# Kernel optimization log

Measured on AMD Instinct MI355X. Metric: run time of the kernel, lower is better.

## Reference

```python
import jax, jax.numpy as jnp
from jax import lax
import numpy as np

SEQ_LEN, INPUT_DIM, NUM_HIDDEN, NUM_CLASSES, BATCH = 512, 64, 128, 10, 1024


def setup_inputs() -> dict:
    key = jax.random.key(0)
    ks = jax.random.split(key, 12)
    bound = float(np.sqrt(1.0 / NUM_HIDDEN))

    def u(k, shape):
        return jax.random.uniform(k, shape, jnp.float32, -bound, bound)

    return {
        "x": jax.random.normal(ks[0], (BATCH, SEQ_LEN, INPUT_DIM), jnp.float32),
        "W_gx": u(ks[1], (INPUT_DIM, NUM_HIDDEN)),
        "W_gh": u(ks[2], (NUM_HIDDEN, NUM_HIDDEN)),
        "W_ix": u(ks[3], (INPUT_DIM, NUM_HIDDEN)),
        "W_ih": u(ks[4], (NUM_HIDDEN, NUM_HIDDEN)),
        "W_fx": u(ks[5], (INPUT_DIM, NUM_HIDDEN)),
        "W_fh": u(ks[6], (NUM_HIDDEN, NUM_HIDDEN)),
        "W_ox": u(ks[7], (INPUT_DIM, NUM_HIDDEN)),
        "W_oh": u(ks[8], (NUM_HIDDEN, NUM_HIDDEN)),
        "W_ph": u(ks[9], (NUM_HIDDEN, NUM_CLASSES)),
        "b_g": jnp.zeros((NUM_HIDDEN,), jnp.float32),
        "b_i": jnp.zeros((NUM_HIDDEN,), jnp.float32),
        "b_f": jnp.ones((NUM_HIDDEN,), jnp.float32),  # forget-gate bias init to 1 as in original
        "b_o": jnp.zeros((NUM_HIDDEN,), jnp.float32),
        "b_p": jnp.zeros((NUM_CLASSES,), jnp.float32),
    }


def reference(x, W_gx, W_gh, W_ix, W_ih, W_fx, W_fh, W_ox, W_oh, W_ph,
              b_g, b_i, b_f, b_o, b_p):
    B, T, D = x.shape
    H = W_gh.shape[0]

    def step(carry, x_t):  # x_t: [B, D]
        h, c = carry
        g = jnp.tanh(x_t @ W_gx + h @ W_gh + b_g)
        i = jax.nn.sigmoid(x_t @ W_ix + h @ W_ih + b_i)
        f = jax.nn.sigmoid(x_t @ W_fx + h @ W_fh + b_f)
        o = jax.nn.sigmoid(x_t @ W_ox + h @ W_oh + b_o)
        c = g * i + c * f
        h = jnp.tanh(c) * o
        return (h, c), None

    h0 = jnp.zeros((B, H), x.dtype)
    c0 = jnp.zeros((B, H), x.dtype)
    (h, c), _ = lax.scan(step, (h0, c0), jnp.swapaxes(x, 0, 1))  # scan over time
    return h @ W_ph + b_p  # [B, num_classes]
```

## Files before the change

### kernel.cpp

```cpp
#include <hip/hip_runtime.h>

#define BATCH 1024
#define TSEQ  512
#define DIN   64
#define H     128
#define NCLS  10
#define BM    16
#define NTHREADS 512

typedef _Float16 h16;
typedef __attribute__((ext_vector_type(4))) _Float16 half4v;
typedef __attribute__((ext_vector_type(8))) _Float16 half8v;
typedef __attribute__((ext_vector_type(4))) float f32x4;

__device__ __forceinline__ int stg_addr(int m, int k) {
    const int kg = k >> 3;
    return (((kg << 4) + (m ^ (kg & 7))) << 3) + (k & 7);
}

__device__ __forceinline__ half4v pack4(float a, float b, float c, float d) {
    half4v v;
    v[0] = (h16)a; v[1] = (h16)b; v[2] = (h16)c; v[3] = (h16)d;
    return v;
}

__device__ __forceinline__ float sig_f(float x) {
    return __builtin_amdgcn_rcpf(1.f + __builtin_amdgcn_exp2f(x * -1.4426950408889634f));
}
__device__ __forceinline__ float tanh_f(float x) {
    float t = __builtin_amdgcn_rcpf(1.f + __builtin_amdgcn_exp2f(x * -2.8853900817779268f));
    return __builtin_fmaf(2.f, t, -1.f);
}

__global__ __launch_bounds__(NTHREADS, 2)
void lstm_persist(const float* __restrict__ x,
                  const float* __restrict__ Wgx, const float* __restrict__ Wgh,
                  const float* __restrict__ Wix, const float* __restrict__ Wih,
                  const float* __restrict__ Wfx, const float* __restrict__ Wfh,
                  const float* __restrict__ Wox, const float* __restrict__ Woh,
                  const float* __restrict__ Wph,
                  const float* __restrict__ bg, const float* __restrict__ bi,
                  const float* __restrict__ bfg, const float* __restrict__ bo,
                  const float* __restrict__ bp,
                  float* __restrict__ out)
{
    __shared__ __align__(16) h16 hbuf[2][H * BM];
    __shared__ __align__(16) h16 xbuf[2][DIN * BM];

    const int tid  = threadIdx.x;
    const int wave = tid >> 6;
    const int lane = tid & 63;
    const int grp  = lane >> 4;
    const int ln   = lane & 15;
    const int b0   = blockIdx.x * BM;
    const int n    = (wave << 4) + ln;

    half8v bx[4][2];
    half8v bh[4][4];
    {
        const float* WX[4] = {Wgx, Wix, Wfx, Wox};
        const float* WH[4] = {Wgh, Wih, Wfh, Woh};
        #pragma unroll
        for (int G = 0; G < 4; ++G) {
            #pragma unroll
            for (int s = 0; s < 2; ++s) {
                half8v v;
                #pragma unroll
                for (int j = 0; j < 8; ++j)
                    v[j] = (h16)WX[G][(32*s + 8*grp + j) * H + n];
                bx[G][s] = v;
            }
            #pragma unroll
            for (int s = 0; s < 4; ++s) {
                half8v v;
                #pragma unroll
                for (int j = 0; j < 8; ++j)
                    v[j] = (h16)WH[G][(32*s + 8*grp + j) * H + n];
                bh[G][s] = v;
            }
        }
    }
    f32x4 bias_c[4];
    {
        const float bv[4] = {bg[n], bi[n], bfg[n], bo[n]};
        #pragma unroll
        for (int G = 0; G < 4; ++G)
            bias_c[G] = (f32x4){bv[G], bv[G], bv[G], bv[G]};
    }

    *(half4v*)&hbuf[0][tid << 2] = (half4v)0;

    const int xm  = tid >> 4;
    const int xk0 = (tid & 15) << 2;
    const int xwr = stg_addr(xm, xk0);
    const float* xrow = x + (size_t)(b0 + xm) * TSEQ * DIN + xk0;

    f32x4 xhold = {0.f, 0.f, 0.f, 0.f};
    f32x4 xnew  = {0.f, 0.f, 0.f, 0.f};
    if (tid < 256) {
        f32x4 x0 = *(const f32x4*)xrow;
        *(half4v*)&xbuf[0][xwr] = pack4(x0[0], x0[1], x0[2], x0[3]);
        xhold = *(const f32x4*)(xrow + DIN);
        xnew  = xhold;
    }

    int hwr[4];
    #pragma unroll
    for (int r = 0; r < 4; ++r) hwr[r] = stg_addr((grp << 2) + r, n);

    f32x4 cstate = {0.f, 0.f, 0.f, 0.f};

    #pragma unroll 2
    for (int t = 0; t < TSEQ; ++t) {
        const int p = t & 1;
        __syncthreads();

        if (tid < 256 && t + 2 < TSEQ)
            xnew = *(const f32x4*)(xrow + (size_t)(t + 2) * DIN);

        half8v ax0 = *(const half8v*)&xbuf[p][stg_addr(ln,      8 * grp)];
        half8v ax1 = *(const half8v*)&xbuf[p][stg_addr(ln, 32 + 8 * grp)];
        half8v ah0 = *(const half8v*)&hbuf[p][stg_addr(ln,      8 * grp)];
        half8v ah1 = *(const half8v*)&hbuf[p][stg_addr(ln, 32 + 8 * grp)];
        half8v ah2 = *(const half8v*)&hbuf[p][stg_addr(ln, 64 + 8 * grp)];
        half8v ah3 = *(const half8v*)&hbuf[p][stg_addr(ln, 96 + 8 * grp)];

        f32x4 acc[4];
        #pragma unroll
        for (int G = 0; G < 4; ++G) {
            f32x4 a = __builtin_amdgcn_mfma_f32_16x16x32_f16(ax0, bx[G][0], bias_c[G], 0, 0, 0);
            a = __builtin_amdgcn_mfma_f32_16x16x32_f16(ax1, bx[G][1], a, 0, 0, 0);
            a = __builtin_amdgcn_mfma_f32_16x16x32_f16(ah0, bh[G][0], a, 0, 0, 0);
            a = __builtin_amdgcn_mfma_f32_16x16x32_f16(ah1, bh[G][1], a, 0, 0, 0);
            a = __builtin_amdgcn_mfma_f32_16x16x32_f16(ah2, bh[G][2], a, 0, 0, 0);
            a = __builtin_amdgcn_mfma_f32_16x16x32_f16(ah3, bh[G][3], a, 0, 0, 0);
            acc[G] = a;
        }

        if (tid < 256)
            *(half4v*)&xbuf[p ^ 1][xwr] = pack4(xhold[0], xhold[1], xhold[2], xhold[3]);
        xhold = xnew;

        f32x4 hv;
        #pragma unroll
        for (int r = 0; r < 4; ++r) {
            float gv = tanh_f(acc[0][r]);
            float iv = sig_f(acc[1][r]);
            float fv = sig_f(acc[2][r]);
            float ov = sig_f(acc[3][r]);
            float c  = __builtin_fmaf(cstate[r], fv, gv * iv);
            cstate[r] = c;
            hv[r] = tanh_f(c) * ov;
        }

        h16* hw = hbuf[p ^ 1];
        #pragma unroll
        for (int r = 0; r < 4; ++r)
            hw[hwr[r]] = (h16)hv[r];
    }

    __syncthreads();
    if (tid < BM * NCLS) {
        const int m = tid / NCLS;
        const int cls = tid - m * NCLS;
        float s = bp[cls];
        #pragma unroll 8
        for (int k = 0; k < H; ++k) {
            float hvv = (float)hbuf[0][stg_addr(m, k)];
            s += hvv * Wph[k * NCLS + cls];
        }
        out[(size_t)(b0 + m) * NCLS + cls] = s;
    }
}

extern "C" void kernel_launch(void* const* d_in, const int* in_sizes, int n_in,
                              void* d_out, int out_size, void* d_ws, size_t ws_size,
                              hipStream_t stream) {
    (void)in_sizes; (void)n_in; (void)d_ws; (void)ws_size; (void)out_size;
    lstm_persist<<<dim3(BATCH / BM), dim3(NTHREADS), 0, stream>>>(
        (const float*)d_in[0],
        (const float*)d_in[1], (const float*)d_in[2],
        (const float*)d_in[3], (const float*)d_in[4],
        (const float*)d_in[5], (const float*)d_in[6],
        (const float*)d_in[7], (const float*)d_in[8],
        (const float*)d_in[9],
        (const float*)d_in[10], (const float*)d_in[11],
        (const float*)d_in[12], (const float*)d_in[13],
        (const float*)d_in[14],
        (float*)d_out);
}
```

Measured before the change: 451.1 us.

## Load x directly into MFMA fragments and precompute next step's input projection

Drops the shared-memory x staging buffer. Each lane now loads its own x fragment from global memory and packs it to fp16, and the x-projection MFMAs for step t+1 are issued during step t using double accumulators. This takes the input projection off the recurrent critical path. Gate weights and biases are also pre-scaled by the -log2(e) factors so the activations skip one multiply each. The cost is redundant global loads of x across the 8 waves, and fp16 rounding of the scaled weights changes numerics slightly.

```diff
diff --git a/kernel.cpp b/kernel.cpp
--- a/kernel.cpp
+++ b/kernel.cpp
@@ -18,19 +18,19 @@
     return (((kg << 4) + (m ^ (kg & 7))) << 3) + (k & 7);
 }
 
-__device__ __forceinline__ half4v pack4(float a, float b, float c, float d) {
-    half4v v;
-    v[0] = (h16)a; v[1] = (h16)b; v[2] = (h16)c; v[3] = (h16)d;
+__device__ __forceinline__ half8v pack8(f32x4 a, f32x4 b) {
+    half8v v;
+    v[0] = (h16)a[0]; v[1] = (h16)a[1]; v[2] = (h16)a[2]; v[3] = (h16)a[3];
+    v[4] = (h16)b[0]; v[5] = (h16)b[1]; v[6] = (h16)b[2]; v[7] = (h16)b[3];
     return v;
 }
 
-__device__ __forceinline__ float sig_f(float x) {
-    return __builtin_amdgcn_rcpf(1.f + __builtin_amdgcn_exp2f(x * -1.4426950408889634f));
-}
-__device__ __forceinline__ float tanh_f(float x) {
-    float t = __builtin_amdgcn_rcpf(1.f + __builtin_amdgcn_exp2f(x * -2.8853900817779268f));
-    return __builtin_fmaf(2.f, t, -1.f);
-}
+__device__ __forceinline__ float sigm_pre(float y) {
+    return __builtin_amdgcn_rcpf(1.f + __builtin_amdgcn_exp2f(y));
+}
+
+#define SCALE_G (-2.8853900817779268f)
+#define SCALE_S (-1.4426950408889634f)
 
 __global__ __launch_bounds__(NTHREADS, 2)
 void lstm_persist(const float* __restrict__ x,
@@ -45,7 +45,6 @@
                   float* __restrict__ out)
 {
     __shared__ __align__(16) h16 hbuf[2][H * BM];
-    __shared__ __align__(16) h16 xbuf[2][DIN * BM];
 
     const int tid  = threadIdx.x;
     const int wave = tid >> 6;
@@ -57,9 +56,12 @@
 
     half8v bx[4][2];
     half8v bh[4][4];
+    f32x4  bias_c[4];
     {
         const float* WX[4] = {Wgx, Wix, Wfx, Wox};
         const float* WH[4] = {Wgh, Wih, Wfh, Woh};
+        const float* BB[4] = {bg, bi, bfg, bo};
+        const float  SC[4] = {SCALE_G, SCALE_S, SCALE_S, SCALE_S};
         #pragma unroll
         for (int G = 0; G < 4; ++G) {
             #pragma unroll
@@ -67,7 +69,7 @@
                 half8v v;
                 #pragma unroll
                 for (int j = 0; j < 8; ++j)
-                    v[j] = (h16)WX[G][(32*s + 8*grp + j) * H + n];
+                    v[j] = (h16)(WX[G][(32*s + 8*grp + j) * H + n] * SC[G]);
                 bx[G][s] = v;
             }
             #pragma unroll
@@ -75,89 +77,102 @@
                 half8v v;
                 #pragma unroll
                 for (int j = 0; j < 8; ++j)
-                    v[j] = (h16)WH[G][(32*s + 8*grp + j) * H + n];
+                    v[j] = (h16)(WH[G][(32*s + 8*grp + j) * H + n] * SC[G]);
                 bh[G][s] = v;
             }
+            const float bb = BB[G][n] * SC[G];
+            bias_c[G] = (f32x4){bb, bb, bb, bb};
         }
     }
-    f32x4 bias_c[4];
-    {
-        const float bv[4] = {bg[n], bi[n], bfg[n], bo[n]};
-        #pragma unroll
-        for (int G = 0; G < 4; ++G)
-            bias_c[G] = (f32x4){bv[G], bv[G], bv[G], bv[G]};
-    }
 
     *(half4v*)&hbuf[0][tid << 2] = (half4v)0;
 
-    const int xm  = tid >> 4;
-    const int xk0 = (tid & 15) << 2;
-    const int xwr = stg_addr(xm, xk0);
-    const float* xrow = x + (size_t)(b0 + xm) * TSEQ * DIN + xk0;
-
-    f32x4 xhold = {0.f, 0.f, 0.f, 0.f};
-    f32x4 xnew  = {0.f, 0.f, 0.f, 0.f};
-    if (tid < 256) {
-        f32x4 x0 = *(const f32x4*)xrow;
-        *(half4v*)&xbuf[0][xwr] = pack4(x0[0], x0[1], x0[2], x0[3]);
-        xhold = *(const f32x4*)(xrow + DIN);
-        xnew  = xhold;
-    }
-
+    const int ha0 = stg_addr(ln,      8 * grp);
+    const int ha1 = stg_addr(ln, 32 + 8 * grp);
+    const int ha2 = stg_addr(ln, 64 + 8 * grp);
+    const int ha3 = stg_addr(ln, 96 + 8 * grp);
     int hwr[4];
     #pragma unroll
     for (int r = 0; r < 4; ++r) hwr[r] = stg_addr((grp << 2) + r, n);
 
-    f32x4 cstate = {0.f, 0.f, 0.f, 0.f};
-
-    #pragma unroll 2
-    for (int t = 0; t < TSEQ; ++t) {
-        const int p = t & 1;
-        __syncthreads();
-
-        if (tid < 256 && t + 2 < TSEQ)
-            xnew = *(const f32x4*)(xrow + (size_t)(t + 2) * DIN);
-
-        half8v ax0 = *(const half8v*)&xbuf[p][stg_addr(ln,      8 * grp)];
-        half8v ax1 = *(const half8v*)&xbuf[p][stg_addr(ln, 32 + 8 * grp)];
-        half8v ah0 = *(const half8v*)&hbuf[p][stg_addr(ln,      8 * grp)];
-        half8v ah1 = *(const half8v*)&hbuf[p][stg_addr(ln, 32 + 8 * grp)];
-        half8v ah2 = *(const half8v*)&hbuf[p][stg_addr(ln, 64 + 8 * grp)];
-        half8v ah3 = *(const half8v*)&hbuf[p][stg_addr(ln, 96 + 8 * grp)];
-
-        f32x4 acc[4];
+    const float* xbase = x + ((size_t)(b0 + ln) * TSEQ) * DIN + (grp << 3);
+
+    f32x4 accA[4], accB[4];
+    {
+        f32x4 a0 = *(const f32x4*)(xbase);
+        f32x4 a1 = *(const f32x4*)(xbase + 4);
+        f32x4 a2 = *(const f32x4*)(xbase + 32);
+        f32x4 a3 = *(const f32x4*)(xbase + 36);
+        half8v xf0 = pack8(a0, a1);
+        half8v xf1 = pack8(a2, a3);
         #pragma unroll
         for (int G = 0; G < 4; ++G) {
-            f32x4 a = __builtin_amdgcn_mfma_f32_16x16x32_f16(ax0, bx[G][0], bias_c[G], 0, 0, 0);
-            a = __builtin_amdgcn_mfma_f32_16x16x32_f16(ax1, bx[G][1], a, 0, 0, 0);
-            a = __builtin_amdgcn_mfma_f32_16x16x32_f16(ah0, bh[G][0], a, 0, 0, 0);
-            a = __builtin_amdgcn_mfma_f32_16x16x32_f16(ah1, bh[G][1], a, 0, 0, 0);
-            a = __builtin_amdgcn_mfma_f32_16x16x32_f16(ah2, bh[G][2], a, 0, 0, 0);
-            a = __builtin_amdgcn_mfma_f32_16x16x32_f16(ah3, bh[G][3], a, 0, 0, 0);
-            acc[G] = a;
+            accA[G] = __builtin_amdgcn_mfma_f32_16x16x32_f16(xf0, bx[G][0], bias_c[G], 0, 0, 0);
+            accA[G] = __builtin_amdgcn_mfma_f32_16x16x32_f16(xf1, bx[G][1], accA[G], 0, 0, 0);
         }
-
-        if (tid < 256)
-            *(half4v*)&xbuf[p ^ 1][xwr] = pack4(xhold[0], xhold[1], xhold[2], xhold[3]);
-        xhold = xnew;
-
-        f32x4 hv;
-        #pragma unroll
-        for (int r = 0; r < 4; ++r) {
-            float gv = tanh_f(acc[0][r]);
-            float iv = sig_f(acc[1][r]);
-            float fv = sig_f(acc[2][r]);
-            float ov = sig_f(acc[3][r]);
-            float c  = __builtin_fmaf(cstate[r], fv, gv * iv);
-            cstate[r] = c;
-            hv[r] = tanh_f(c) * ov;
-        }
-
-        h16* hw = hbuf[p ^ 1];
-        #pragma unroll
-        for (int r = 0; r < 4; ++r)
-            hw[hwr[r]] = (h16)hv[r];
-    }
+    }
+    const float* xptr = xbase + DIN;
+    f32x4 xr0 = *(const f32x4*)(xptr);
+    f32x4 xr1 = *(const f32x4*)(xptr + 4);
+    f32x4 xr2 = *(const f32x4*)(xptr + 32);
+    f32x4 xr3 = *(const f32x4*)(xptr + 36);
+    xptr += DIN;
+
+    f32x4 cstate = {0.f, 0.f, 0.f, 0.f};
+
+#define STEP(p_, tcur, ACCC, ACCN)                                              \
+  {                                                                             \
+    __syncthreads();                                                            \
+    half8v ah0 = *(const half8v*)&hbuf[p_][ha0];                                \
+    half8v ah1 = *(const half8v*)&hbuf[p_][ha1];                                \
+    half8v ah2 = *(const half8v*)&hbuf[p_][ha2];                                \
+    half8v ah3 = *(const half8v*)&hbuf[p_][ha3];                                \
+    _Pragma("unroll")                                                           \
+    for (int G = 0; G < 4; ++G) {                                               \
+        ACCC[G] = __builtin_amdgcn_mfma_f32_16x16x32_f16(ah0, bh[G][0], ACCC[G], 0, 0, 0); \
+        ACCC[G] = __builtin_amdgcn_mfma_f32_16x16x32_f16(ah1, bh[G][1], ACCC[G], 0, 0, 0); \
+        ACCC[G] = __builtin_amdgcn_mfma_f32_16x16x32_f16(ah2, bh[G][2], ACCC[G], 0, 0, 0); \
+        ACCC[G] = __builtin_amdgcn_mfma_f32_16x16x32_f16(ah3, bh[G][3], ACCC[G], 0, 0, 0); \
+    }                                                                           \
+                             \
+    half8v xf0 = pack8(xr0, xr1);                                               \
+    half8v xf1 = pack8(xr2, xr3);                                               \
+                   \
+    xr0 = *(const f32x4*)(xptr);                                                \
+    xr1 = *(const f32x4*)(xptr + 4);                                            \
+    xr2 = *(const f32x4*)(xptr + 32);                                           \
+    xr3 = *(const f32x4*)(xptr + 36);                                           \
+    if ((tcur) + 3 < TSEQ) xptr += DIN;                                         \
+                   \
+    _Pragma("unroll")                                                           \
+    for (int G = 0; G < 4; ++G) {                                               \
+        ACCN[G] = __builtin_amdgcn_mfma_f32_16x16x32_f16(xf0, bx[G][0], bias_c[G], 0, 0, 0); \
+        ACCN[G] = __builtin_amdgcn_mfma_f32_16x16x32_f16(xf1, bx[G][1], ACCN[G], 0, 0, 0); \
+    }                                                                           \
+                    \
+    f32x4 hv;                                                                   \
+    _Pragma("unroll")                                                           \
+    for (int r = 0; r < 4; ++r) {                                               \
+        float gv = __builtin_fmaf(2.f, sigm_pre(ACCC[0][r]), -1.f);             \
+        float iv = sigm_pre(ACCC[1][r]);                                        \
+        float fv = sigm_pre(ACCC[2][r]);                                        \
+        float ov = sigm_pre(ACCC[3][r]);                                        \
+        float c  = __builtin_fmaf(cstate[r], fv, gv * iv);                      \
+        cstate[r] = c;                                                          \
+        float tc = __builtin_fmaf(2.f, sigm_pre(c * SCALE_G), -1.f);            \
+        hv[r] = tc * ov;                                                        \
+    }                                                                           \
+    h16* hw = hbuf[p_ ^ 1];                                                     \
+    _Pragma("unroll")                                                           \
+    for (int r = 0; r < 4; ++r)                                                 \
+        hw[hwr[r]] = (h16)hv[r];                                                \
+  }
+
+    for (int t = 0; t < TSEQ; t += 2) {
+        STEP(0, t,     accA, accB)
+        STEP(1, t + 1, accB, accA)
+    }
+#undef STEP
 
     __syncthreads();
     if (tid < BM * NCLS) {
```

Measured after the change: 530.7 us. 17.6% more time.
